# Performance work log

Measured on AMD Instinct MI355X. Metric: run time of the kernel, lower is better.

Reference implementation:

```python
import jax, jax.numpy as jnp
import numpy as np
from jax import lax

B, TX, RX, RATE, DIMZ, HID, DIRS = 8192, 32, 32, 2, 64, 128, 2
S, FEAT = 2 * TX, 2 * TX + 1
BN_EPS = 1e-5
GD_STEP = 1e-6   # hardcoded in original forward
GD_ITERS = 10    # hardcoded in original forward


def setup_inputs() -> dict:
    key = jax.random.key(0)
    ks = jax.random.split(key, 9)
    sc = 1.0 / np.sqrt(HID)
    return {
        "y": jax.random.normal(ks[0], (B, 2 * RX), jnp.float32),
        "H": jax.random.normal(ks[1], (B, 2 * RX, 2 * TX), jnp.float32),
        "x_raw": jax.random.randint(ks[2], (B, 2 * TX, 1), 0, 2 ** RATE).astype(jnp.float32),
        "gru_w_ih": jax.random.uniform(ks[3], (DIRS, 3 * HID, FEAT), jnp.float32, -sc, sc),
        "gru_w_hh": jax.random.uniform(ks[4], (DIRS, 3 * HID, HID), jnp.float32, -sc, sc),
        "gru_b_ih": jax.random.uniform(ks[5], (DIRS, 3 * HID), jnp.float32, -sc, sc),
        "gru_b_hh": jax.random.uniform(ks[6], (DIRS, 3 * HID), jnp.float32, -sc, sc),
        "w_Wz": jax.random.normal(ks[7], (DIMZ, DIRS * HID), jnp.float32),
        "w_Wx": jax.random.normal(ks[8], (DIMZ, DIRS * HID), jnp.float32),
        "bn_gamma": jnp.ones((2 * TX,), jnp.float32),
        "bn_beta": jnp.zeros((2 * TX,), jnp.float32),
        "step_size": 1,
        "iterations": 10,
    }


def _gru_dir(x_seq, wih, whh, bih, bhh):
    # x_seq: (S, B, F); PyTorch GRU cell equations
    xg = jnp.einsum('sbf,gf->sbg', x_seq, wih) + bih  # (S, B, 3H)

    def step(h, xg_t):
        hg = h @ whh.T + bhh
        xr, xz, xn = jnp.split(xg_t, 3, axis=-1)
        hr, hz, hn = jnp.split(hg, 3, axis=-1)
        r = jax.nn.sigmoid(xr + hr)
        z = jax.nn.sigmoid(xz + hz)
        n = jnp.tanh(xn + r * hn)
        h = (1.0 - z) * n + z * h
        return h, h

    h0 = jnp.zeros((x_seq.shape[1], whh.shape[1]), x_seq.dtype)
    _, out = lax.scan(step, h0, xg)
    return out  # (S, B, H)


def reference(y, H, x_raw, gru_w_ih, gru_w_hh, gru_b_ih, gru_b_hh,
              w_Wz, w_Wx, bn_gamma, bn_beta, step_size, iterations):
    # Hty: (B, 2tx, 1), HtH: (B, 2tx, 2tx)
    Hty = jnp.einsum('brt,br->bt', H, y)[..., None]
    HtH = jnp.einsum('brt,bru->btu', H, H)

    # BatchNorm1d over channel dim 2tx (stats over batch and last dim)
    feats = jnp.concatenate([HtH, Hty], axis=-1)  # (B, 2tx, 2tx+1)
    mu = feats.mean(axis=(0, 2), keepdims=True)
    var = feats.var(axis=(0, 2), keepdims=True)
    feats = (feats - mu) / jnp.sqrt(var + BN_EPS)
    feats = feats * bn_gamma[None, :, None] + bn_beta[None, :, None]

    # bidirectional GRU over seq dim (seq_len = 2tx)
    x_seq = jnp.transpose(feats, (1, 0, 2))  # (S, B, F)
    fwd = _gru_dir(x_seq, gru_w_ih[0], gru_w_hh[0], gru_b_ih[0], gru_b_hh[0])
    bwd = _gru_dir(x_seq[::-1], gru_w_ih[1], gru_w_hh[1], gru_b_ih[1], gru_b_hh[1])[::-1]
    go = jnp.concatenate([fwd, bwd], axis=-1)  # (S, B, 2H)

    w_z = jnp.transpose(go @ w_Wz.T, (1, 2, 0))  # (B, dim_z, S)
    w_x = jnp.transpose(go @ w_Wx.T, (1, 0, 2))  # (B, S, dim_z)

    x_hat0 = 2.0 * x_raw - (2.0 ** RATE) + 1.0  # QAM symbols
    z0 = w_z @ x_hat0  # (B, dim_z, 1)

    # gradient-descent loop (step_size/iterations args ignored, as in source)
    wxt = jnp.swapaxes(w_x, 1, 2)        # (B, dim_z, 2tx)
    wxt_hty = wxt @ Hty                  # (B, dim_z, 1)
    whhw = wxt @ (HtH @ w_x)             # (B, dim_z, dim_z)
    two_step = 2.0 * GD_STEP

    def gd(zh, _):
        return zh + two_step * (wxt_hty - whhw @ zh), None

    z_hat, _ = lax.scan(gd, z0, None, length=GD_ITERS)
    return w_x @ z_hat  # (B, 2tx, 1)
```

## Files before the change

### kernel.cpp

```cpp
#include <hip/hip_runtime.h>
#include <math.h>


typedef __attribute__((ext_vector_type(8))) short s8v;
typedef __attribute__((ext_vector_type(4))) float f4v;

__device__ __forceinline__ short f2bf(float x) {
  unsigned u = __float_as_uint(x);
  u += 0x7fffu + ((u >> 16) & 1u);
  return (short)(u >> 16);
}
__device__ __forceinline__ float bf2f(short h) {
  return __uint_as_float(((unsigned)(unsigned short)h) << 16);
}
__device__ __forceinline__ void fma4(float4& c, float a, const float4 w) {
  c.x += a*w.x; c.y += a*w.y; c.z += a*w.z; c.w += a*w.w;
}
__device__ __forceinline__ float vget(const float4& v, int i) { return ((const float*)&v)[i]; }

__device__ __forceinline__ void gload16(const void* g, void* l) {
  __builtin_amdgcn_global_load_lds(
      (const __attribute__((address_space(1))) void*)g,
      (__attribute__((address_space(3))) void*)l, 16, 0, 0);
}

#define MFMA(A, B, C) __builtin_amdgcn_mfma_f32_16x16x32_bf16((A), (B), (C), 0, 0, 0)

__global__ __launch_bounds__(256) void k_feats(
    const float* __restrict__ Hm, const float* __restrict__ y,
    short* __restrict__ fragX, float* __restrict__ htyU, float* __restrict__ bnacc)
{
  __shared__ __align__(16) float Hl[64][68];
  __shared__ float yl[64];
  __shared__ float s1[64], s2[64];
  const int b = blockIdx.x;
  const int tid = threadIdx.x;
  const float* Hb = Hm + (size_t)b*4096;
  for (int i = tid; i < 4096; i += 256) Hl[i>>6][i&63] = Hb[i];
  if (tid < 64) { yl[tid] = y[b*64+tid]; s1[tid] = 0.f; s2[tid] = 0.f; }
  __syncthreads();

  if (tid < 64) {
    float acc = 0.f;
    for (int r = 0; r < 64; ++r) acc += Hl[r][tid]*yl[r];
    htyU[tid*8192 + b] = acc;
    atomicAdd(&s1[tid], acc);
    atomicAdd(&s2[tid], acc*acc);
  }
  const int tg = tid & 15, ug = tid >> 4;
  float4 acc4[4];
  acc4[0]=acc4[1]=acc4[2]=acc4[3]=make_float4(0.f,0.f,0.f,0.f);
  for (int r = 0; r < 64; ++r) {
    const float4 tv = *(const float4*)&Hl[r][4*tg];
    const float4 uv = *(const float4*)&Hl[r][4*ug];
    #pragma unroll
    for (int tt=0;tt<4;++tt) fma4(acc4[tt], vget(tv,tt), uv);
  }
  const int mt   = (b >> 4) & 3;
  const int brow = b & 15;
  const int u0   = 4*ug;
  short* fbase = fragX + (size_t)(b >> 6)*64*8192
               + (mt*2 + (u0 >> 5))*512 + (brow + 16*((u0 >> 3) & 3))*8 + (u0 & 7);
  #pragma unroll
  for (int tt=0;tt<4;++tt) {
    const int t = 4*tg+tt;
    float sv=0.f, sq=0.f;
    short hib[4], lob[4];
    #pragma unroll
    for (int uu=0;uu<4;++uu) {
      const float v = vget(acc4[tt],uu);
      const short hi = f2bf(v);
      hib[uu] = hi; lob[uu] = f2bf(v - bf2f(hi));
      sv += v; sq += v*v;
    }
    short* dst = fbase + (size_t)t*8192;
    *(short4*)dst          = make_short4(hib[0],hib[1],hib[2],hib[3]);
    *(short4*)(dst + 4096) = make_short4(lob[0],lob[1],lob[2],lob[3]);
    sv += __shfl_down(sv,32); sq += __shfl_down(sq,32);
    sv += __shfl_down(sv,16); sq += __shfl_down(sq,16);
    if ((tid & 63) < 16) { atomicAdd(&s1[t], sv); atomicAdd(&s2[t], sq); }
  }
  __syncthreads();
  if (tid < 64) {
    atomicAdd(&bnacc[tid*16],      s1[tid]);
    atomicAdd(&bnacc[(64+tid)*16], s2[tid]);
  }
}

__global__ void k_bnfin(const float* __restrict__ bnacc, const float* __restrict__ gam,
                        const float* __restrict__ bet, float* __restrict__ bnac)
{
  const int t = threadIdx.x;
  if (t < 64) {
    const float inv = 1.f/532480.f;
    const float mu  = bnacc[t*16]*inv;
    const float var = bnacc[(64+t)*16]*inv - mu*mu;
    const float a = gam[t]*rsqrtf(var + 1e-5f);
    bnac[t] = a;
    bnac[64+t] = bet[t] - mu*a;
  }
}

__global__ __launch_bounds__(256) void k_prep(
    const float* __restrict__ wih, const float* __restrict__ whh,
    const float* __restrict__ Wz, const float* __restrict__ Wx,
    short* __restrict__ Wg, short* __restrict__ W2g, float* __restrict__ rowsum)
{
  const int i = blockIdx.x*256 + threadIdx.x;
  if (i < 294912) {
    const int dd = i / 147456, r = i % 147456;
    const int sp = r / 73728, r2 = r % 73728;
    const int chunk = r2 / 512, e = r2 % 512;
    const int lane = e >> 3, ii = e & 7;
    const int nt = chunk / 6, kt = chunk % 6;
    const int n = nt*16 + (lane & 15);
    const int k = kt*32 + (lane >> 4)*8 + ii;
    const float v = (k < 64) ? wih[dd*24960 + n*65 + k]
                             : whh[dd*49152 + n*128 + (k - 64)];
    const short hi = f2bf(v);
    Wg[i] = sp ? f2bf(v - bf2f(hi)) : hi;
  } else if (i < 360448) {
    const int t = i - 294912;
    const int dd = t / 32768, r = t % 32768;
    const int sp = r / 16384, r2 = r % 16384;
    const int chunk = r2 / 512, e = r2 % 512;
    const int lane = e >> 3, ii = e & 7;
    const int nt2 = chunk / 4, kt = chunk % 4;
    const int n2 = nt2*16 + (lane & 15);
    const int k = kt*32 + (lane >> 4)*8 + ii;
    const float v = (n2 < 64) ? Wx[n2*256 + dd*128 + k]
                              : Wz[(n2 - 64)*256 + dd*128 + k];
    const short hi = f2bf(v);
    W2g[t] = sp ? f2bf(v - bf2f(hi)) : hi;
  } else if (i < 361216) {
    const int t = i - 360448;
    const int dd = t / 384, g = t % 384;
    float ssum = 0.f;
    for (int f = 0; f < 65; ++f) ssum += wih[dd*24960 + g*65 + f];
    rowsum[t] = ssum;
  }
}

__global__ __launch_bounds__(512, 4) void k_scan(
    const short* __restrict__ fragX, const float* __restrict__ htyU,
    const float* __restrict__ xraw,
    const short* __restrict__ Wg, const short* __restrict__ W2g,
    const float* __restrict__ bih, const float* __restrict__ bhh,
    const float* __restrict__ rowsum, const float* __restrict__ bnac,
    const float* __restrict__ wih,
    float* __restrict__ wx_out, float* __restrict__ z0_out)
{
  __shared__ __align__(16) short Axb[8192];
  __shared__ __align__(16) short Ahb[16384];
  __shared__ __align__(16) float xl[64][36];
  __shared__ __align__(16) float gcl[1536];
  __shared__ __align__(16) float z0l[32][68];
  __shared__ float bna[128];

  const int tid = threadIdx.x;
  const int l   = tid & 63;
  const int w   = __builtin_amdgcn_readfirstlane(tid >> 6);
  const int tile = blockIdx.x >> 1, d = blockIdx.x & 1;
  const int b0  = tile * 32;
  const int T64 = tile >> 1, hh = tile & 1;
  const int l15 = l & 15, lq = l >> 4;
  const int j   = 16*w + l15;
  const int zcol = 16*(w & 3) + l15;

  const short* Wgd = Wg  + d*147456;
  const short* W2d = W2g + d*32768;
  float* wxo = wx_out + (size_t)d * (8192ull*4096ull);
  float* z0o = z0_out + (size_t)d * (8192ull*64ull);

  const int wbG = w*3072 + l*8;
  const int wbP = w*2048 + l*8;

  const int hw_base = (j >> 5)*512 + ((j >> 3) & 3)*128 + (j & 7);

  const int c_sp  = w >> 2, c_mtl = (w >> 1) & 1, c_kt = w & 1;
  const size_t choff = (size_t)c_sp*8192 + (size_t)(2*(2*hh + c_mtl) + c_kt)*1024;
  const char* fragT = (const char*)fragX + (size_t)T64*1048576ull;

  for (int i = tid; i < 16384; i += 512) Ahb[i] = 0;
  for (int i = tid; i < 2048; i += 512) {
    const int bl = i >> 6, s = i & 63;
    xl[s][bl] = 2.f*xraw[(size_t)(b0 + bl)*64 + s] - 3.f;
  }
  if (tid < 128) {
    const int jj = tid;
    float* g = &gcl[jj*12];
    g[0] = rowsum[d*384 + jj];
    g[1] = rowsum[d*384 + 128 + jj];
    g[2] = rowsum[d*384 + 256 + jj];
    g[3] = bih[d*384 + jj]       + bhh[d*384 + jj];
    g[4] = bih[d*384 + 128 + jj] + bhh[d*384 + 128 + jj];
    g[5] = bih[d*384 + 256 + jj];
    g[6] = bhh[d*384 + 256 + jj];
    g[7] = wih[d*24960 + jj*65 + 64];
    g[8] = wih[d*24960 + (128 + jj)*65 + 64];
    g[9] = wih[d*24960 + (256 + jj)*65 + 64];
    g[10] = 0.f; g[11] = 0.f;
  }
  for (int i = tid; i < 32*68; i += 512) ((float*)z0l)[i] = 0.f;
  if (tid < 128) bna[tid] = bnac[tid];

  f4v hprev[2];
  hprev[0] = (f4v)0.f; hprev[1] = (f4v)0.f;

  {
    const int s0 = d ? 63 : 0;
    gload16(fragT + (size_t)s0*16384 + choff + l*16, (char*)Axb + w*1024);
  }
  __syncthreads();

  for (int it = 0; it < 64; ++it) {
    const int s  = d ? 63 - it : it;
    const int sn = (it < 63) ? (d ? s - 1 : s + 1) : s;

    int lz = 0;
    asm volatile("" : "+v"(lz));
    const short* Wv  = Wgd + lz;
    const short* W2v = W2d + lz;

    const short* AxR = Axb + ((it & 1) << 12);
    char*        AxW = (char*)Axb + (((it + 1) & 1) << 13);
    const short* AhR = Ahb + (((it + 1) & 1) << 13);
    short*       AhW = Ahb + ((it & 1) << 13);

    gload16(fragT + (size_t)sn*16384 + choff + l*16, AxW + w*1024);

    const float a_s = bna[s], c_s = bna[64 + s];
    const volatile float* gj = gcl + j*12;
    const float crK  = c_s*gj[0] + gj[3];
    const float czK  = c_s*gj[1] + gj[4];
    const float cnK  = c_s*gj[2] + gj[5];
    const float BHN  = gj[6];
    const float w64r = gj[7], w64z = gj[8], w64n = gj[9];

    const float4 hty0 = *(const float4*)&htyU[s*8192 + b0 + lq*4];
    const float4 hty1 = *(const float4*)&htyU[s*8192 + b0 + 16 + lq*4];

    f4v Crx[2], Czx[2], Cnx[2], Crh[2], Czh[2], Cnh[2];
    #pragma unroll
    for (int m = 0; m < 2; ++m) {
      Crx[m]=(f4v)0.f; Czx[m]=(f4v)0.f; Cnx[m]=(f4v)0.f;
      Crh[m]=(f4v)0.f; Czh[m]=(f4v)0.f; Cnh[m]=(f4v)0.f;
    }
    #pragma unroll
    for (int kt = 0; kt < 6; ++kt) {
      const s8v bRh = *(const s8v*)&Wv[wbG + kt*512];
      const s8v bRl = *(const s8v*)&Wv[wbG + 73728 + kt*512];
      const s8v bZh = *(const s8v*)&Wv[wbG + 24576 + kt*512];
      const s8v bZl = *(const s8v*)&Wv[wbG + 98304 + kt*512];
      const s8v bNh = *(const s8v*)&Wv[wbG + 49152 + kt*512];
      const s8v bNl = *(const s8v*)&Wv[wbG + 122880 + kt*512];
      if (kt < 2) {
        #pragma unroll
        for (int m = 0; m < 2; ++m) {
          const s8v ah = *(const s8v*)&AxR[m*1024 + kt*512 + l*8];
          const s8v al = *(const s8v*)&AxR[2048 + m*1024 + kt*512 + l*8];
          Crx[m]=MFMA(ah,bRh,Crx[m]); Crx[m]=MFMA(ah,bRl,Crx[m]); Crx[m]=MFMA(al,bRh,Crx[m]);
          Czx[m]=MFMA(ah,bZh,Czx[m]); Czx[m]=MFMA(ah,bZl,Czx[m]); Czx[m]=MFMA(al,bZh,Czx[m]);
          Cnx[m]=MFMA(ah,bNh,Cnx[m]); Cnx[m]=MFMA(ah,bNl,Cnx[m]); Cnx[m]=MFMA(al,bNh,Cnx[m]);
        }
      } else {
        const int kh = kt - 2;
        #pragma unroll
        for (int m = 0; m < 2; ++m) {
          const s8v ah = *(const s8v*)&AhR[m*2048 + kh*512 + l*8];
          const s8v al = *(const s8v*)&AhR[4096 + m*2048 + kh*512 + l*8];
          Crh[m]=MFMA(ah,bRh,Crh[m]); Crh[m]=MFMA(ah,bRl,Crh[m]); Crh[m]=MFMA(al,bRh,Crh[m]);
          Czh[m]=MFMA(ah,bZh,Czh[m]); Czh[m]=MFMA(ah,bZl,Czh[m]); Czh[m]=MFMA(al,bZh,Czh[m]);
          Cnh[m]=MFMA(ah,bNh,Cnh[m]); Cnh[m]=MFMA(ah,bNl,Cnh[m]); Cnh[m]=MFMA(al,bNh,Cnh[m]);
        }
      }
    }

    #pragma unroll
    for (int m = 0; m < 2; ++m) {
      const float4 av4 = m ? hty1 : hty0;
      f4v av; av[0]=av4.x; av[1]=av4.y; av[2]=av4.z; av[3]=av4.w;
      const f4v crx = Crx[m] + av * w64r;
      const f4v czx = Czx[m] + av * w64z;
      const f4v cnx = Cnx[m] + av * w64n;
      #pragma unroll
      for (int e = 0; e < 4; ++e) {
        const float rr  = 1.f/(1.f + __expf(-(a_s*crx[e] + Crh[m][e] + crK)));
        const float zz  = 1.f/(1.f + __expf(-(a_s*czx[e] + Czh[m][e] + czK)));
        const float pre = a_s*cnx[e] + cnK + rr*(Cnh[m][e] + BHN);
        const float ax2 = fabsf(pre);
        const float ee  = __expf(-2.f*ax2);
        const float nn  = copysignf((1.f - ee)/(1.f + ee), pre);
        hprev[m][e] = (1.f - zz)*nn + zz*hprev[m][e];
      }
    }

    #pragma unroll
    for (int m = 0; m < 2; ++m)
      #pragma unroll
      for (int e = 0; e < 4; ++e) {
        const float hv = hprev[m][e];
        const short hi = f2bf(hv);
        const int ad = m*2048 + hw_base + (lq*4 + e)*8;
        AhW[ad] = hi;
        AhW[4096 + ad] = f2bf(hv - bf2f(hi));
      }
    __syncthreads();

    f4v Cp[2]; Cp[0] = (f4v)0.f; Cp[1] = (f4v)0.f;
    #pragma unroll
    for (int kt = 0; kt < 4; ++kt) {
      const s8v bPh = *(const s8v*)&W2v[wbP + kt*512];
      const s8v bPl = *(const s8v*)&W2v[wbP + 16384 + kt*512];
      #pragma unroll
      for (int m = 0; m < 2; ++m) {
        const s8v ah = *(const s8v*)&AhW[m*2048 + kt*512 + l*8];
        const s8v al = *(const s8v*)&AhW[4096 + m*2048 + kt*512 + l*8];
        Cp[m]=MFMA(ah,bPh,Cp[m]); Cp[m]=MFMA(ah,bPl,Cp[m]); Cp[m]=MFMA(al,bPh,Cp[m]);
      }
    }
    #pragma unroll
    for (int m = 0; m < 2; ++m) {
      if (w < 4) {
        #pragma unroll
        for (int e = 0; e < 4; ++e)
          wxo[(size_t)(b0 + m*16 + lq*4 + e)*4096 + s*64 + 16*w + l15] = Cp[m][e];
      } else {
        #pragma unroll
        for (int e = 0; e < 4; ++e) {
          const int bl = m*16 + lq*4 + e;
          z0l[bl][zcol] += xl[s][bl] * Cp[m][e];
        }
      }
    }
  }
  if (w >= 4) {
    #pragma unroll
    for (int m = 0; m < 2; ++m)
      #pragma unroll
      for (int e = 0; e < 4; ++e) {
        const int bl = m*16 + lq*4 + e;
        z0o[(size_t)(b0 + bl)*64 + zcol] = z0l[bl][zcol];
      }
  }
}

__global__ __launch_bounds__(256) void k_gd(
    const float* __restrict__ Hm, const float* __restrict__ y,
    const float* __restrict__ wxf, const float* __restrict__ wxb,
    const float* __restrict__ z0f, const float* __restrict__ z0b,
    float* __restrict__ out)
{
  __shared__ __align__(16) float Hl[64][68];
  __shared__ __align__(16) float wx[64][68];
  __shared__ __align__(16) float tmp[64][68];
  __shared__ float yl[64], wh[64], zv[64];
  const int b = blockIdx.x;
  const int tid = threadIdx.x;
  const float* Hb = Hm + (size_t)b*4096;
  for (int i = tid; i < 4096; i += 256) {
    Hl[i>>6][i&63] = Hb[i];
    wx[i>>6][i&63] = wxf[(size_t)b*4096 + i] + wxb[(size_t)b*4096 + i];
  }
  if (tid < 64) {
    yl[tid] = y[b*64+tid];
    zv[tid] = z0f[(size_t)b*64+tid] + z0b[(size_t)b*64+tid];
  }
  __syncthreads();
  const int zq = tid & 15, tq = tid >> 4;
  #pragma unroll
  for (int rr = 0; rr < 4; ++rr) {
    const int r = 4*tq + rr;
    float4 a = make_float4(0.f,0.f,0.f,0.f);
    for (int t = 0; t < 64; ++t) fma4(a, Hl[r][t], *(const float4*)&wx[t][4*zq]);
    *(float4*)&tmp[r][4*zq] = a;
  }
  __syncthreads();
  float (*ww)[68] = Hl;
  #pragma unroll
  for (int ii = 0; ii < 4; ++ii) {
    const int zi = 4*tq + ii;
    float4 a = make_float4(0.f,0.f,0.f,0.f);
    for (int r = 0; r < 64; ++r) fma4(a, tmp[r][zi], *(const float4*)&tmp[r][4*zq]);
    *(float4*)&ww[zi][4*zq] = a;
  }
  if (tid < 64) {
    float acc = 0.f;
    for (int r = 0; r < 64; ++r) acc += tmp[r][tid]*yl[r];
    wh[tid] = acc;
  }
  __syncthreads();
  for (int itr = 0; itr < 10; ++itr) {
    float nz = 0.f;
    if (tid < 64) {
      float mv = 0.f;
      for (int k2 = 0; k2 < 64; ++k2) mv += ww[tid][k2]*zv[k2];
      nz = zv[tid] + 2e-6f*(wh[tid] - mv);
    }
    __syncthreads();
    if (tid < 64) zv[tid] = nz;
    __syncthreads();
  }
  if (tid < 64) {
    float o = 0.f;
    for (int z2 = 0; z2 < 64; ++z2) o += wx[tid][z2]*zv[z2];
    out[(size_t)b*64 + tid] = o;
  }
}

extern "C" void kernel_launch(void* const* d_in, const int* in_sizes, int n_in,
                              void* d_out, int out_size, void* d_ws, size_t ws_size,
                              hipStream_t stream)
{
  const float* y    = (const float*)d_in[0];
  const float* Hm   = (const float*)d_in[1];
  const float* xraw = (const float*)d_in[2];
  const float* wih  = (const float*)d_in[3];
  const float* whh  = (const float*)d_in[4];
  const float* bih  = (const float*)d_in[5];
  const float* bhh  = (const float*)d_in[6];
  const float* Wz   = (const float*)d_in[7];
  const float* Wx   = (const float*)d_in[8];
  const float* gam  = (const float*)d_in[9];
  const float* bet  = (const float*)d_in[10];
  float* out = (float*)d_out;
  float* ws  = (float*)d_ws;

  float* wxf   = ws;
  float* wxb   = wxf + 33554432ull;
  float* z0f   = wxb + 33554432ull;
  float* z0b   = z0f + 524288ull;
  float* htyU  = z0b + 524288ull;
  float* rows  = htyU + 524288ull;
  float* bnacc = rows + 768ull;
  float* bnac  = bnacc + 2048ull;
  short* Wgs   = (short*)(bnac + 128ull);
  short* W2gs  = Wgs + 294912ull;
  short* fragX = W2gs + 65536ull;

  hipMemsetAsync(bnacc, 0, 2048*sizeof(float), stream);
  k_feats <<<8192, 256, 0, stream>>>(Hm, y, fragX, htyU, bnacc);
  k_prep  <<<1412, 256, 0, stream>>>(wih, whh, Wz, Wx, Wgs, W2gs, rows);
  k_bnfin <<<1, 64, 0, stream>>>(bnacc, gam, bet, bnac);
  k_scan  <<<512, 512, 0, stream>>>(fragX, htyU, xraw, Wgs, W2gs,
                                    bih, bhh, rows, bnac, wih, wxf, z0f);
  k_gd    <<<8192, 256, 0, stream>>>(Hm, y, wxf, wxb, z0f, z0b, out);
}
```

Baseline: 1.868 ms.

## Defer output projection by one step and fuse into GRU hidden MFMA loop

The per-step projection of the hidden state onto Wz/Wx (Cp MFMAs) is moved out of its own phase after the barrier. It now runs inside the next timestep's hidden-gate MFMA loop, reusing the already-loaded A fragments of h_{t-1}, and a tail block handles the final step. This removes the second pass over the hidden-state LDS fragments and shortens the serial per-step critical path, at the cost of more live accumulator registers. The block-index mapping also changes so that the two directions occupy separate halves of the grid instead of interleaving.

```diff
diff --git a/kernel.cpp b/kernel.cpp
--- a/kernel.cpp
+++ b/kernel.cpp
@@ -160,7 +160,7 @@
   const int tid = threadIdx.x;
   const int l   = tid & 63;
   const int w   = __builtin_amdgcn_readfirstlane(tid >> 6);
-  const int tile = blockIdx.x >> 1, d = blockIdx.x & 1;
+  const int tile = blockIdx.x & 255, d = blockIdx.x >> 8;
   const int b0  = tile * 32;
   const int T64 = tile >> 1, hh = tile & 1;
   const int l15 = l & 15, lq = l >> 4;
@@ -216,6 +216,7 @@
   for (int it = 0; it < 64; ++it) {
     const int s  = d ? 63 - it : it;
     const int sn = (it < 63) ? (d ? s - 1 : s + 1) : s;
+    const int sp_prev = d ? s + 1 : s - 1;
 
     int lz = 0;
     asm volatile("" : "+v"(lz));
@@ -240,11 +241,11 @@
     const float4 hty0 = *(const float4*)&htyU[s*8192 + b0 + lq*4];
     const float4 hty1 = *(const float4*)&htyU[s*8192 + b0 + 16 + lq*4];
 
-    f4v Crx[2], Czx[2], Cnx[2], Crh[2], Czh[2], Cnh[2];
+    f4v Crx[2], Czx[2], Cnx[2], Crh[2], Czh[2], Cnh[2], Cp[2];
     #pragma unroll
     for (int m = 0; m < 2; ++m) {
       Crx[m]=(f4v)0.f; Czx[m]=(f4v)0.f; Cnx[m]=(f4v)0.f;
-      Crh[m]=(f4v)0.f; Czh[m]=(f4v)0.f; Cnh[m]=(f4v)0.f;
+      Crh[m]=(f4v)0.f; Czh[m]=(f4v)0.f; Cnh[m]=(f4v)0.f; Cp[m]=(f4v)0.f;
     }
     #pragma unroll
     for (int kt = 0; kt < 6; ++kt) {
@@ -265,6 +266,8 @@
         }
       } else {
         const int kh = kt - 2;
+        const s8v bPh = *(const s8v*)&W2v[wbP + kh*512];
+        const s8v bPl = *(const s8v*)&W2v[wbP + 16384 + kh*512];
         #pragma unroll
         for (int m = 0; m < 2; ++m) {
           const s8v ah = *(const s8v*)&AhR[m*2048 + kh*512 + l*8];
@@ -272,6 +275,24 @@
           Crh[m]=MFMA(ah,bRh,Crh[m]); Crh[m]=MFMA(ah,bRl,Crh[m]); Crh[m]=MFMA(al,bRh,Crh[m]);
           Czh[m]=MFMA(ah,bZh,Czh[m]); Czh[m]=MFMA(ah,bZl,Czh[m]); Czh[m]=MFMA(al,bZh,Czh[m]);
           Cnh[m]=MFMA(ah,bNh,Cnh[m]); Cnh[m]=MFMA(ah,bNl,Cnh[m]); Cnh[m]=MFMA(al,bNh,Cnh[m]);
+          Cp[m]=MFMA(ah,bPh,Cp[m]);   Cp[m]=MFMA(ah,bPl,Cp[m]);   Cp[m]=MFMA(al,bPh,Cp[m]);
+        }
+      }
+    }
+
+    if (it > 0) {
+      #pragma unroll
+      for (int m = 0; m < 2; ++m) {
+        if (w < 4) {
+          #pragma unroll
+          for (int e = 0; e < 4; ++e)
+            wxo[(size_t)(b0 + m*16 + lq*4 + e)*4096 + sp_prev*64 + 16*w + l15] = Cp[m][e];
+        } else {
+          #pragma unroll
+          for (int e = 0; e < 4; ++e) {
+            const int bl = m*16 + lq*4 + e;
+            z0l[bl][zcol] += xl[sp_prev][bl] * Cp[m][e];
+          }
         }
       }
     }
@@ -306,7 +327,14 @@
         AhW[4096 + ad] = f2bf(hv - bf2f(hi));
       }
     __syncthreads();
-
+  }
+
+  {
+    const short* AhF = Ahb + 8192;
+    const int sl = d ? 0 : 63;
+    int lz = 0;
+    asm volatile("" : "+v"(lz));
+    const short* W2v = W2d + lz;
     f4v Cp[2]; Cp[0] = (f4v)0.f; Cp[1] = (f4v)0.f;
     #pragma unroll
     for (int kt = 0; kt < 4; ++kt) {
@@ -314,8 +342,8 @@
       const s8v bPl = *(const s8v*)&W2v[wbP + 16384 + kt*512];
       #pragma unroll
       for (int m = 0; m < 2; ++m) {
-        const s8v ah = *(const s8v*)&AhW[m*2048 + kt*512 + l*8];
-        const s8v al = *(const s8v*)&AhW[4096 + m*2048 + kt*512 + l*8];
+        const s8v ah = *(const s8v*)&AhF[m*2048 + kt*512 + l*8];
+        const s8v al = *(const s8v*)&AhF[4096 + m*2048 + kt*512 + l*8];
         Cp[m]=MFMA(ah,bPh,Cp[m]); Cp[m]=MFMA(ah,bPl,Cp[m]); Cp[m]=MFMA(al,bPh,Cp[m]);
       }
     }
@@ -324,12 +352,12 @@
       if (w < 4) {
         #pragma unroll
         for (int e = 0; e < 4; ++e)
-          wxo[(size_t)(b0 + m*16 + lq*4 + e)*4096 + s*64 + 16*w + l15] = Cp[m][e];
+          wxo[(size_t)(b0 + m*16 + lq*4 + e)*4096 + sl*64 + 16*w + l15] = Cp[m][e];
       } else {
         #pragma unroll
         for (int e = 0; e < 4; ++e) {
           const int bl = m*16 + lq*4 + e;
-          z0l[bl][zcol] += xl[s][bl] * Cp[m][e];
+          z0l[bl][zcol] += xl[sl][bl] * Cp[m][e];
         }
       }
     }
```

New measurement: 1.982 ms. +6.1%, slower.
